# Optimization experiments

Hardware: AMD Instinct MI355X
Metric: run time of the kernel (lower is better)

The kernel has to match this reference:

```python
import jax, jax.numpy as jnp
from jax import lax
import numpy as np

B, CIN, COUT, WDIM, SIN, K = 8, 512, 512, 512, 64, 3
UP, DOWN, TAPS = 2, 2, 12
PX0, PX1, PY0, PY1 = 9, 8, 9, 8  # from StyleGAN3 padding formula for these rates
CLAMP, SLOPE = 256.0, 0.2
GAIN = float(np.sqrt(2.0))
FS_TMP, CUTOFF, HALFW = 128.0, 16.0, 16.0
DN = ('NCHW', 'OIHW', 'NCHW')


def _kaiser_beta(a):
    if a > 50.0:
        return 0.1102 * (a - 8.7)
    if a > 21.0:
        return 0.5842 * (a - 21.0) ** 0.4 + 0.07886 * (a - 21.0)
    return 0.0


def _firwin(numtaps, cutoff, width, fs):
    # replicates scipy.signal.firwin(numtaps, cutoff, width=width, fs=fs)
    nyq = fs / 2.0
    atten = 2.285 * (numtaps - 1) * np.pi * (width / nyq) + 7.95
    beta = _kaiser_beta(atten)
    win = np.kaiser(numtaps, beta)
    m = np.arange(numtaps) - (numtaps - 1) / 2.0
    fc = cutoff / nyq
    h = fc * np.sinc(fc * m) * win
    h /= h.sum()
    return h.astype(np.float32)


def setup_inputs() -> dict:
    key = jax.random.key(0)
    ks = jax.random.split(key, 4)
    f = jnp.asarray(_firwin(TAPS, CUTOFF, 2.0 * HALFW, FS_TMP))
    return {
        'x': jax.random.normal(ks[0], (B, CIN, SIN, SIN), jnp.float32),
        'w': jax.random.normal(ks[1], (B, WDIM), jnp.float32),
        'affine_w': jax.random.normal(ks[2], (CIN, WDIM), jnp.float32),
        'affine_b': jnp.ones((CIN,), jnp.float32),  # bias_init=1
        'conv_w': jax.random.normal(ks[3], (COUT, CIN, K, K), jnp.float32),
        'conv_b': jnp.zeros((COUT,), jnp.float32),
        'up_filter': f,
        'down_filter': f,  # same cutoff/width/fs for in and out here
    }


def _depthwise(x, f1d, axis, stride=1, pad=(0, 0), lhs_dil=1):
    # separable depthwise FIR along one spatial axis (axis 2 = H, 3 = W)
    C, t = x.shape[1], f1d.shape[0]
    if axis == 2:
        k = jnp.broadcast_to(f1d.reshape(1, 1, t, 1), (C, 1, t, 1))
        return lax.conv_general_dilated(x, k, (stride, 1), [pad, (0, 0)],
                                        lhs_dilation=(lhs_dil, 1),
                                        feature_group_count=C, dimension_numbers=DN)
    k = jnp.broadcast_to(f1d.reshape(1, 1, 1, t), (C, 1, 1, t))
    return lax.conv_general_dilated(x, k, (1, stride), [(0, 0), pad],
                                    lhs_dilation=(1, lhs_dil),
                                    feature_group_count=C, dimension_numbers=DN)


def reference(x, w, affine_w, affine_b, conv_w, conv_b, up_filter, down_filter):
    # --- affine: FullyConnectedLayer(w_dim, in_channels, bias_init=1) ---
    styles = w @ (affine_w.T * (1.0 / np.sqrt(WDIM))) + affine_b  # [B, CIN]
    # --- modulated_conv2d with demodulation (input_gain = ema.rsqrt() = 1) ---
    wt = conv_w * lax.rsqrt(jnp.mean(conv_w ** 2, axis=(1, 2, 3), keepdims=True))
    s = styles * lax.rsqrt(jnp.mean(styles ** 2))
    ww = wt[None] * s[:, None, :, None, None]                     # [B,COUT,CIN,K,K]
    ww = ww * lax.rsqrt(jnp.sum(ww ** 2, axis=(2, 3, 4)) + 1e-8)[:, :, None, None, None]
    conv1 = lambda xi, wi: lax.conv_general_dilated(
        xi[None], wi, (1, 1), [(K - 1, K - 1)] * 2, dimension_numbers=DN)[0]
    x = jax.vmap(conv1)(x, ww)                                    # [B,COUT,66,66]
    # --- filtered_lrelu: bias -> upfirdn(up) -> lrelu*gain, clamp -> upfirdn(down) ---
    x = x + conv_b[None, :, None, None]
    fu = up_filter[::-1] * UP  # flip_filter=False; per-pass gain = up (total up^2)
    x = _depthwise(x, fu, 2, pad=(PY0, PY1 + UP - 1), lhs_dil=UP)
    x = _depthwise(x, fu, 3, pad=(PX0, PX1 + UP - 1), lhs_dil=UP)  # [B,COUT,138,138]
    x = jnp.clip(jnp.where(x >= 0, x, SLOPE * x) * GAIN, -CLAMP, CLAMP)
    fd = down_filter[::-1]
    x = _depthwise(x, fd, 2, stride=DOWN)
    x = _depthwise(x, fd, 3, stride=DOWN)                          # [B,COUT,64,64]
    return x
```

## Files before the change

kernel.cpp:

```cpp
#include <hip/hip_runtime.h>

typedef __attribute__((ext_vector_type(4))) float floatx4;
typedef __attribute__((ext_vector_type(8))) short short8;

#define AS1(p) ((const __attribute__((address_space(1))) unsigned int*)(p))
#define AS3(p) ((__attribute__((address_space(3))) unsigned int*)(p))

static __device__ __forceinline__ void async16(const void* g, void* l) {
  __builtin_amdgcn_global_load_lds(AS1(g), AS3(l), 16, 0, 0);
}

static __device__ __forceinline__ unsigned short f2bf(float f) {
  unsigned u = __float_as_uint(f);
  unsigned r = u + 0x7FFFu + ((u >> 16) & 1u);
  return (unsigned short)(r >> 16);
}
static __device__ __forceinline__ float bf2f(unsigned short h) {
  return __uint_as_float(((unsigned)h) << 16);
}
static __device__ __forceinline__ float bf_lo(unsigned u) { return __uint_as_float(u << 16); }
static __device__ __forceinline__ float bf_hi(unsigned u) { return __uint_as_float(u & 0xFFFF0000u); }

static __device__ __forceinline__ float actf(float v) {
  float a = v >= 0.f ? v : 0.2f * v;
  a *= 1.41421356237309515f;
  return fminf(fmaxf(a, -256.f), 256.f);
}

__global__ void k_styles(const float* __restrict__ w, const float* __restrict__ aw,
                         const float* __restrict__ ab, float* __restrict__ styles) {
  int t = blockIdx.x * 256 + threadIdx.x;
  int b = t >> 9, c = t & 511;
  float acc = 0.f;
  for (int d = 0; d < 512; ++d) acc += w[b * 512 + d] * aw[c * 512 + d];
  styles[t] = acc * 0.04419417382415922f + ab[c];
}

__global__ void k_msr(const float* __restrict__ styles, float* __restrict__ msr) {
  __shared__ float red[256];
  float acc = 0.f;
  for (int i = threadIdx.x; i < 4096; i += 256) { float v = styles[i]; acc += v * v; }
  red[threadIdx.x] = acc; __syncthreads();
  for (int s = 128; s > 0; s >>= 1) {
    if ((int)threadIdx.x < s) red[threadIdx.x] += red[threadIdx.x + s];
    __syncthreads();
  }
  if (threadIdx.x == 0) *msr = rsqrtf(red[0] / 4096.0f);
}

__global__ void k_wstat(const float* __restrict__ cw, float* __restrict__ t, float* __restrict__ q) {
  int o = blockIdx.x, tid = threadIdx.x;
  __shared__ float red[256];
  float tot = 0.f;
  for (int i = tid; i < 512; i += 256) {
    const float* p = cw + ((size_t)o * 512 + i) * 9;
    float s = 0.f;
#pragma unroll
    for (int k = 0; k < 9; ++k) s += p[k] * p[k];
    q[o * 512 + i] = s;
    tot += s;
  }
  red[tid] = tot; __syncthreads();
  for (int s2 = 128; s2 > 0; s2 >>= 1) {
    if (tid < s2) red[tid] += red[tid + s2];
    __syncthreads();
  }
  if (tid == 0) t[o] = rsqrtf(red[0] / 4608.0f);
}

__global__ void k_dmod(const float* __restrict__ styles, const float* __restrict__ msr,
                       const float* __restrict__ t, const float* __restrict__ q,
                       float* __restrict__ g) {
  int idx = blockIdx.x * 256 + threadIdx.x;
  int b = idx >> 9, o = idx & 511;
  float m = *msr;
  float acc = 0.f;
  for (int i = 0; i < 512; ++i) {
    float s = styles[b * 512 + i] * m;
    acc += s * s * q[o * 512 + i];
  }
  float to = t[o];
  g[idx] = to * rsqrtf(to * to * acc + 1e-8f);
}

__global__ __launch_bounds__(256) void k_wpack(const float* __restrict__ cw,
                                               const float* __restrict__ styles,
                                               const float* __restrict__ msr,
                                               const float* __restrict__ g,
                                               unsigned short* __restrict__ wbf2) {
  __shared__ float raw[512][11];
  int o = blockIdx.x, tid = threadIdx.x;
  for (int i = tid; i < 512; i += 256) {
    const float* p = cw + ((size_t)o * 512 + i) * 9;
#pragma unroll
    for (int k = 0; k < 9; ++k) raw[i][k] = p[k];
  }
  __syncthreads();
  float m = *msr;
  const int nb = o >> 7, wn = (o >> 6) & 1, ni = (o >> 4) & 3, ol = o & 15;
  for (int b = 0; b < 8; ++b) {
    float gg = g[b * 512 + o];
    const size_t base_bo = ((size_t)(b * 4 + nb) * 2 + wn);
    for (int f = tid; f < 9 * 512; f += 256) {
      int s = f >> 9, i = f & 511;
      int ic = i >> 5, qq = (i >> 3) & 3, j = i & 7;
      float v = raw[i][s] * gg * (styles[b * 512 + i] * m);
      size_t idx = ((((base_bo * 9 + s) * 16 + ic) * 4 + ni) * 512) + (qq * 16 + ol) * 8 + j;
      wbf2[idx] = f2bf(v);
    }
  }
}

__global__ __launch_bounds__(256) void k_xpack(const float* __restrict__ x,
                                               unsigned short* __restrict__ xp) {
  __shared__ float tile[64][65];
  int Y = blockIdx.x, cc0 = blockIdx.y * 64, b = blockIdx.z;
  int tid = threadIdx.x;
  int yy = Y - 2;
  bool valid = (yy >= 0 && yy < 64);
  if (valid) {
    for (int it = 0; it < 16; ++it) {
      int f = it * 256 + tid;
      int cc = f >> 6, xx = f & 63;
      tile[xx][cc] = x[(((size_t)b * 512 + cc0 + cc) * 64 + yy) * 64 + xx];
    }
  }
  __syncthreads();
  for (int it = 0; it < 17; ++it) {
    int f = it * 256 + tid;
    int X = f >> 6, cc = f & 63;
    int xx = X - 2;
    float v = (valid && xx >= 0 && xx < 64) ? tile[xx][cc] : 0.f;
    xp[(((size_t)b * 68 + Y) * 68 + X) * 512 + cc0 + cc] = f2bf(v);
  }
}

__global__ __launch_bounds__(256, 2) void k_conv(const unsigned short* __restrict__ xp,
                                                 const unsigned short* __restrict__ wbf2,
                                                 const float* __restrict__ cb,
                                                 float* __restrict__ y) {
  __shared__ __align__(16) unsigned short lds[24576];
  const int tid = threadIdx.x;
  const int w = tid >> 6, lane = tid & 63;
  const int wm = w & 1, wn = w >> 1;
  const int q = lane >> 4, ln = lane & 15;

  const int xcd = blockIdx.x & 7;
  const int slot = blockIdx.x >> 3;
  const int combo = xcd * 4 + slot / 35;
  const int mt = slot % 35;
  const int nt = combo & 3;
  const int b = combo >> 2;
  const int m0 = mt * 128, n0 = nt * 128;
  const int oy0 = m0 / 66;

  const unsigned short* xpb = xp + (size_t)b * (68 * 68 * 512);

  size_t gof_p[6];
#pragma unroll
  for (int i = 0; i < 6; ++i) {
    int pv = w * 96 + i * 16 + (lane >> 2);
    int pve = pv < 339 ? pv : 339;
    int r = pve / 68, px = pve - r * 68;
    int Y = oy0 + r; if (Y > 67) Y = 67;
    int ch = ((lane & 3) ^ ((pve >> 1) & 3)) * 8;
    gof_p[i] = (size_t)(Y * 68 + px) * 512 + ch;
  }

  int pvA[4];
#pragma unroll
  for (int mi = 0; mi < 4; ++mi) {
    int p = m0 + wm * 64 + mi * 16 + ln; if (p > 4355) p = 4355;
    int oy = p / 66, ox = p - oy * 66;
    pvA[mi] = (oy - oy0) * 68 + ox;
  }

  const unsigned short* wB = wbf2 + (((size_t)(b * 4 + nt) * 2 + wn) * 294912) + (size_t)lane * 8;

  floatx4 acc[4][4];
#pragma unroll
  for (int i = 0; i < 4; ++i)
#pragma unroll
    for (int j = 0; j < 4; ++j) acc[i][j] = (floatx4){0.f, 0.f, 0.f, 0.f};

  unsigned short* pat0 = lds;
  unsigned short* pat1 = lds + 12288;

#pragma unroll
  for (int i = 0; i < 6; ++i)
    async16(xpb + gof_p[i], pat0 + (w * 96 + i * 16) * 32);

  short8 bF[4];
#pragma unroll
  for (int ni = 0; ni < 4; ++ni)
    bF[ni] = *(const short8*)(wB + ni * 512);

  for (int ic = 0; ic < 16; ++ic) {
    asm volatile("s_waitcnt vmcnt(0)" ::: "memory");
    asm volatile("s_barrier" ::: "memory");
    const unsigned short* pb = (ic & 1) ? pat1 : pat0;
    unsigned short* pn = (ic & 1) ? pat0 : pat1;
    const size_t pchan = (size_t)(ic + 1) * 32;
#pragma unroll
    for (int s = 0; s < 9; ++s) {
      if (s >= 1 && s <= 6 && ic < 15)
        async16(xpb + gof_p[s - 1] + pchan, pn + (w * 96 + (s - 1) * 16) * 32);
      const int sn = (s < 8) ? s + 1 : 0;
      const int icn = (s < 8) ? ic : (ic < 15 ? ic + 1 : 15);
      const unsigned short* wBn = wB + ((size_t)sn * 16 + icn) * 2048;
      short8 bN[4];
#pragma unroll
      for (int ni = 0; ni < 4; ++ni) bN[ni] = *(const short8*)(wBn + ni * 512);
      const int d = (s / 3) * 68 + (s % 3);
      short8 aF[4];
#pragma unroll
      for (int mi = 0; mi < 4; ++mi) {
        int pv = pvA[mi] + d;
        int off = pv * 32 + ((q ^ ((pv >> 1) & 3)) << 3);
        aF[mi] = *(const short8*)(pb + off);
      }
#pragma unroll
      for (int mi = 0; mi < 4; ++mi)
#pragma unroll
        for (int ni = 0; ni < 4; ++ni)
          acc[mi][ni] = __builtin_amdgcn_mfma_f32_16x16x32_bf16(aF[mi], bF[ni], acc[mi][ni], 0, 0, 0);
#pragma unroll
      for (int ni = 0; ni < 4; ++ni) bF[ni] = bN[ni];
    }
  }

  __syncthreads();
  float* slab = (float*)lds + w * 2176;
  const int pbase = m0 + wm * 64;
  const bool pok = (pbase + ln * 4) < 4356;
  float cbv[4];
#pragma unroll
  for (int ni = 0; ni < 4; ++ni) cbv[ni] = cb[n0 + wn * 64 + ni * 16 + ln];

#pragma unroll
  for (int pass = 0; pass < 2; ++pass) {
#pragma unroll
    for (int ni2 = 0; ni2 < 2; ++ni2) {
      const int ni = pass * 2 + ni2;
#pragma unroll
      for (int mi = 0; mi < 4; ++mi) {
        float4 v;
        v.x = acc[mi][ni][0] + cbv[ni];
        v.y = acc[mi][ni][1] + cbv[ni];
        v.z = acc[mi][ni][2] + cbv[ni];
        v.w = acc[mi][ni][3] + cbv[ni];
        *(float4*)&slab[(ni2 * 16 + ln) * 68 + mi * 16 + q * 4] = v;
      }
    }
#pragma unroll
    for (int i = 0; i < 8; ++i) {
      const int orow = i * 4 + q;
      const int o = n0 + wn * 64 + pass * 32 + orow;
      if (pok) {
        float4 vv = *(const float4*)&slab[orow * 68 + ln * 4];
        *(float4*)&y[((size_t)b * 512 + o) * 4356 + pbase + ln * 4] = vv;
      }
    }
  }
}

__global__ __launch_bounds__(256) void k_updown(const float* __restrict__ yg,
                                                const float* __restrict__ uf,
                                                const float* __restrict__ df,
                                                float* __restrict__ out) {
  __shared__ __align__(16) unsigned short t1t2[64 * 144];
  __shared__ __align__(16) unsigned short zbuf[138 * 144];
  const int tid = threadIdx.x;
  const int plane = blockIdx.x;
  const float* yp = yg + (size_t)plane * 4356;
  float fuw[12], fdw[12];
#pragma unroll
  for (int i = 0; i < 12; ++i) { fuw[i] = uf[11 - i] * 2.0f; fdw[i] = df[11 - i]; }

  for (int t = tid; t < 69 * 66; t += 256) {
    int v = t / 66, xx = t - v * 66;
    float ae = 0.f, ao = 0.f;
#pragma unroll
    for (int u = 0; u < 6; ++u) {
      int r = v + u - 4;
      float yv = (r >= 0 && r < 66) ? yp[r * 66 + xx] : 0.f;
      ae += yv * fuw[2 * u + 1];
      ao += yv * fuw[2 * u];
    }
    t1t2[(2 * v) * 66 + xx] = f2bf(ae);
    t1t2[(2 * v + 1) * 66 + xx] = f2bf(ao);
  }
  __syncthreads();

  for (int t = tid; t < 138 * 69; t += 256) {
    int Y = t / 69, h = t - Y * 69;
    float ae = 0.f, ao = 0.f;
#pragma unroll
    for (int u = 0; u < 6; ++u) {
      int c = h + u - 4;
      float tv = (c >= 0 && c < 66) ? bf2f(t1t2[Y * 66 + c]) : 0.f;
      ae += tv * fuw[2 * u + 1];
      ao += tv * fuw[2 * u];
    }
    ae = actf(ae); ao = actf(ao);
    unsigned pack = (unsigned)f2bf(ae) | ((unsigned)f2bf(ao) << 16);
    *(unsigned*)&zbuf[Y * 144 + 2 * h] = pack;
  }
  __syncthreads();

  for (int t = tid; t < 64 * 18; t += 256) {
    int yr = t / 18, cx = t - yr * 18;
    int X0 = cx * 8;
    float acc[8];
#pragma unroll
    for (int e = 0; e < 8; ++e) acc[e] = 0.f;
#pragma unroll
    for (int i = 0; i < 12; ++i) {
      uint4 zv = *(const uint4*)&zbuf[(2 * yr + i) * 144 + X0];
      float c = fdw[i];
      acc[0] += c * bf_lo(zv.x); acc[1] += c * bf_hi(zv.x);
      acc[2] += c * bf_lo(zv.y); acc[3] += c * bf_hi(zv.y);
      acc[4] += c * bf_lo(zv.z); acc[5] += c * bf_hi(zv.z);
      acc[6] += c * bf_lo(zv.w); acc[7] += c * bf_hi(zv.w);
    }
    uint4 st;
    st.x = (unsigned)f2bf(acc[0]) | ((unsigned)f2bf(acc[1]) << 16);
    st.y = (unsigned)f2bf(acc[2]) | ((unsigned)f2bf(acc[3]) << 16);
    st.z = (unsigned)f2bf(acc[4]) | ((unsigned)f2bf(acc[5]) << 16);
    st.w = (unsigned)f2bf(acc[6]) | ((unsigned)f2bf(acc[7]) << 16);
    *(uint4*)&t1t2[yr * 144 + X0] = st;
  }
  __syncthreads();

  for (int t = tid; t < 4096; t += 256) {
    int yr = t >> 6, xx = t & 63;
    float acc = 0.f;
#pragma unroll
    for (int j = 0; j < 12; j += 2) {
      unsigned pv = *(const unsigned*)&t1t2[yr * 144 + 2 * xx + j];
      acc += fdw[j] * bf_lo(pv) + fdw[j + 1] * bf_hi(pv);
    }
    out[(size_t)plane * 4096 + t] = acc;
  }
}

extern "C" void kernel_launch(void* const* d_in, const int* in_sizes, int n_in,
                              void* d_out, int out_size, void* d_ws, size_t ws_size,
                              hipStream_t stream) {
  const float* x  = (const float*)d_in[0];
  const float* w  = (const float*)d_in[1];
  const float* aw = (const float*)d_in[2];
  const float* ab = (const float*)d_in[3];
  const float* cw = (const float*)d_in[4];
  const float* cb = (const float*)d_in[5];
  const float* uf = (const float*)d_in[6];
  const float* df = (const float*)d_in[7];
  float* out = (float*)d_out;
  char* ws = (char*)d_ws;

  float* styles = (float*)(ws + 0);
  float* msr    = (float*)(ws + 16384);
  float* tbuf   = (float*)(ws + 16640);
  float* qbuf   = (float*)(ws + 18688);
  float* gbuf   = (float*)(ws + 1067264);
  unsigned short* xp   = (unsigned short*)(ws + 1083648);
  unsigned short* wbf2 = (unsigned short*)(ws + 38963456);
  float* yb            = (float*)(ws + 76712192);

  k_styles<<<16, 256, 0, stream>>>(w, aw, ab, styles);
  k_msr<<<1, 256, 0, stream>>>(styles, msr);
  k_wstat<<<512, 256, 0, stream>>>(cw, tbuf, qbuf);
  k_dmod<<<16, 256, 0, stream>>>(styles, msr, tbuf, qbuf, gbuf);
  k_wpack<<<512, 256, 0, stream>>>(cw, styles, msr, gbuf, wbf2);
  k_xpack<<<dim3(68, 8, 8), 256, 0, stream>>>(x, xp);
  k_conv<<<1120, 256, 0, stream>>>(xp, wbf2, cb, yb);
  k_updown<<<4096, 256, 0, stream>>>(yb, uf, df, out);
}
```

Measured before the change: 657.5 us.

## Split updown planes into column halves with register-blocked FIR passes

The up/down filter kernel now handles half of each plane's output columns per block, doubling the grid. It stages the input tile in LDS with halo and computes 8 outputs per thread in each FIR pass using vectorized LDS reads. The activation gain is folded into the second up-filter's coefficients. Shared memory per block shrinks, which allows four blocks per CU under the new launch bounds. The cost is redundant halo computation at the column split, plus higher register pressure from the 8-wide accumulators.

```diff
diff --git a/kernel.cpp b/kernel.cpp
--- a/kernel.cpp
+++ b/kernel.cpp
@@ -15,17 +15,17 @@
   unsigned r = u + 0x7FFFu + ((u >> 16) & 1u);
   return (unsigned short)(r >> 16);
 }
+static __device__ __forceinline__ unsigned packbf(float lo, float hi) {
+  unsigned ul = __float_as_uint(lo), uh = __float_as_uint(hi);
+  ul = ul + 0x7FFFu + ((ul >> 16) & 1u);
+  uh = uh + 0x7FFFu + ((uh >> 16) & 1u);
+  return (ul >> 16) | (uh & 0xFFFF0000u);
+}
 static __device__ __forceinline__ float bf2f(unsigned short h) {
   return __uint_as_float(((unsigned)h) << 16);
 }
 static __device__ __forceinline__ float bf_lo(unsigned u) { return __uint_as_float(u << 16); }
 static __device__ __forceinline__ float bf_hi(unsigned u) { return __uint_as_float(u & 0xFFFF0000u); }
-
-static __device__ __forceinline__ float actf(float v) {
-  float a = v >= 0.f ? v : 0.2f * v;
-  a *= 1.41421356237309515f;
-  return fminf(fmaxf(a, -256.f), 256.f);
-}
 
 __global__ void k_styles(const float* __restrict__ w, const float* __restrict__ aw,
                          const float* __restrict__ ab, float* __restrict__ styles) {
@@ -264,59 +264,120 @@
   }
 }
 
-__global__ __launch_bounds__(256) void k_updown(const float* __restrict__ yg,
-                                                const float* __restrict__ uf,
-                                                const float* __restrict__ df,
-                                                float* __restrict__ out) {
-  __shared__ __align__(16) unsigned short t1t2[64 * 144];
-  __shared__ __align__(16) unsigned short zbuf[138 * 144];
+__global__ __launch_bounds__(256, 4) void k_updown(const float* __restrict__ yg,
+                                                   const float* __restrict__ uf,
+                                                   const float* __restrict__ df,
+                                                   float* __restrict__ out) {
+  __shared__ __align__(16) unsigned short zraw[138 * 88];
+  __shared__ __align__(16) unsigned short t1buf[138 * 56];
   const int tid = threadIdx.x;
-  const int plane = blockIdx.x;
+  const int plane = blockIdx.x >> 1;
+  const int s = blockIdx.x & 1;
   const float* yp = yg + (size_t)plane * 4356;
-  float fuw[12], fdw[12];
-#pragma unroll
-  for (int i = 0; i < 12; ++i) { fuw[i] = uf[11 - i] * 2.0f; fdw[i] = df[11 - i]; }
-
-  for (int t = tid; t < 69 * 66; t += 256) {
-    int v = t / 66, xx = t - v * 66;
-    float ae = 0.f, ao = 0.f;
+
+  float fub[12], fuc[12], fdw[12];
+#pragma unroll
+  for (int i = 0; i < 12; ++i) {
+    float u = uf[11 - i] * 2.0f;
+    fub[i] = u;
+    fuc[i] = u * 1.41421356237309515f;
+    fdw[i] = df[11 - i];
+  }
+
+  float* ybuf = (float*)zraw;
+  const int xoff = 32 * s - 4;
+  for (int t = tid; t < 75 * 48; t += 256) {
+    int row = t / 48, col = t - row * 48;
+    int r = row - 4, x = xoff + col;
+    float v = (r >= 0 && r < 66 && x >= 0 && x < 66) ? yp[r * 66 + x] : 0.f;
+    ybuf[t] = v;
+  }
+  __syncthreads();
+
+  for (int t = tid; t < 69 * 6; t += 256) {
+    int v = t / 6, c = t - v * 6;
+    float ae[8], ao[8];
+#pragma unroll
+    for (int e = 0; e < 8; ++e) { ae[e] = 0.f; ao[e] = 0.f; }
 #pragma unroll
     for (int u = 0; u < 6; ++u) {
-      int r = v + u - 4;
-      float yv = (r >= 0 && r < 66) ? yp[r * 66 + xx] : 0.f;
-      ae += yv * fuw[2 * u + 1];
-      ao += yv * fuw[2 * u];
-    }
-    t1t2[(2 * v) * 66 + xx] = f2bf(ae);
-    t1t2[(2 * v + 1) * 66 + xx] = f2bf(ao);
-  }
-  __syncthreads();
-
-  for (int t = tid; t < 138 * 69; t += 256) {
-    int Y = t / 69, h = t - Y * 69;
-    float ae = 0.f, ao = 0.f;
+      const float* yr = &ybuf[(v + u) * 48 + 8 * c];
+      float4 p0 = *(const float4*)yr;
+      float4 p1 = *(const float4*)(yr + 4);
+      float fe = fub[2 * u + 1], fo = fub[2 * u];
+      ae[0] += p0.x * fe; ao[0] += p0.x * fo;
+      ae[1] += p0.y * fe; ao[1] += p0.y * fo;
+      ae[2] += p0.z * fe; ao[2] += p0.z * fo;
+      ae[3] += p0.w * fe; ao[3] += p0.w * fo;
+      ae[4] += p1.x * fe; ao[4] += p1.x * fo;
+      ae[5] += p1.y * fe; ao[5] += p1.y * fo;
+      ae[6] += p1.z * fe; ao[6] += p1.z * fo;
+      ae[7] += p1.w * fe; ao[7] += p1.w * fo;
+    }
+    uint4 se, so;
+    se.x = packbf(ae[0], ae[1]); se.y = packbf(ae[2], ae[3]);
+    se.z = packbf(ae[4], ae[5]); se.w = packbf(ae[6], ae[7]);
+    so.x = packbf(ao[0], ao[1]); so.y = packbf(ao[2], ao[3]);
+    so.z = packbf(ao[4], ao[5]); so.w = packbf(ao[6], ao[7]);
+    *(uint4*)&t1buf[(2 * v) * 56 + 8 * c] = se;
+    *(uint4*)&t1buf[(2 * v + 1) * 56 + 8 * c] = so;
+  }
+  __syncthreads();
+
+  for (int t = tid; t < 138 * 5; t += 256) {
+    int Y = t / 5, k = t - Y * 5;
+    const unsigned short* tr = &t1buf[Y * 56 + 8 * k];
+    uint4 r0 = *(const uint4*)tr;
+    uint4 r1 = *(const uint4*)(tr + 8);
+    float a[14];
+    a[0] = bf_lo(r0.x);  a[1] = bf_hi(r0.x);
+    a[2] = bf_lo(r0.y);  a[3] = bf_hi(r0.y);
+    a[4] = bf_lo(r0.z);  a[5] = bf_hi(r0.z);
+    a[6] = bf_lo(r0.w);  a[7] = bf_hi(r0.w);
+    a[8] = bf_lo(r1.x);  a[9] = bf_hi(r1.x);
+    a[10] = bf_lo(r1.y); a[11] = bf_hi(r1.y);
+    a[12] = bf_lo(r1.z); a[13] = bf_hi(r1.z);
+    float ae[8], ao[8];
+#pragma unroll
+    for (int p = 0; p < 8; ++p) { ae[p] = 0.f; ao[p] = 0.f; }
 #pragma unroll
     for (int u = 0; u < 6; ++u) {
-      int c = h + u - 4;
-      float tv = (c >= 0 && c < 66) ? bf2f(t1t2[Y * 66 + c]) : 0.f;
-      ae += tv * fuw[2 * u + 1];
-      ao += tv * fuw[2 * u];
-    }
-    ae = actf(ae); ao = actf(ao);
-    unsigned pack = (unsigned)f2bf(ae) | ((unsigned)f2bf(ao) << 16);
-    *(unsigned*)&zbuf[Y * 144 + 2 * h] = pack;
-  }
-  __syncthreads();
-
-  for (int t = tid; t < 64 * 18; t += 256) {
-    int yr = t / 18, cx = t - yr * 18;
-    int X0 = cx * 8;
+      float fe = fuc[2 * u + 1], fo = fuc[2 * u];
+#pragma unroll
+      for (int p = 0; p < 8; ++p) {
+        float tv = a[p + u];
+        ae[p] += tv * fe;
+        ao[p] += tv * fo;
+      }
+    }
+    uint4 s0, s1;
+    float ze[8], zo[8];
+#pragma unroll
+    for (int p = 0; p < 8; ++p) {
+      float v0 = fmaxf(ae[p], 0.f) + 0.2f * fminf(ae[p], 0.f);
+      float v1 = fmaxf(ao[p], 0.f) + 0.2f * fminf(ao[p], 0.f);
+      ze[p] = fminf(fmaxf(v0, -256.f), 256.f);
+      zo[p] = fminf(fmaxf(v1, -256.f), 256.f);
+    }
+    s0.x = packbf(ze[0], zo[0]); s0.y = packbf(ze[1], zo[1]);
+    s0.z = packbf(ze[2], zo[2]); s0.w = packbf(ze[3], zo[3]);
+    s1.x = packbf(ze[4], zo[4]); s1.y = packbf(ze[5], zo[5]);
+    s1.z = packbf(ze[6], zo[6]); s1.w = packbf(ze[7], zo[7]);
+    unsigned short* zr = &zraw[Y * 88 + 16 * k];
+    *(uint4*)zr = s0;
+    *(uint4*)(zr + 8) = s1;
+  }
+  __syncthreads();
+
+  unsigned short* t2 = t1buf;
+  for (int t = tid; t < 64 * 10; t += 256) {
+    int yr = t / 10, k = t - yr * 10;
     float acc[8];
 #pragma unroll
     for (int e = 0; e < 8; ++e) acc[e] = 0.f;
 #pragma unroll
     for (int i = 0; i < 12; ++i) {
-      uint4 zv = *(const uint4*)&zbuf[(2 * yr + i) * 144 + X0];
+      uint4 zv = *(const uint4*)&zraw[(2 * yr + i) * 88 + 8 * k];
       float c = fdw[i];
       acc[0] += c * bf_lo(zv.x); acc[1] += c * bf_hi(zv.x);
       acc[2] += c * bf_lo(zv.y); acc[3] += c * bf_hi(zv.y);
@@ -324,23 +385,45 @@
       acc[6] += c * bf_lo(zv.w); acc[7] += c * bf_hi(zv.w);
     }
     uint4 st;
-    st.x = (unsigned)f2bf(acc[0]) | ((unsigned)f2bf(acc[1]) << 16);
-    st.y = (unsigned)f2bf(acc[2]) | ((unsigned)f2bf(acc[3]) << 16);
-    st.z = (unsigned)f2bf(acc[4]) | ((unsigned)f2bf(acc[5]) << 16);
-    st.w = (unsigned)f2bf(acc[6]) | ((unsigned)f2bf(acc[7]) << 16);
-    *(uint4*)&t1t2[yr * 144 + X0] = st;
-  }
-  __syncthreads();
-
-  for (int t = tid; t < 4096; t += 256) {
-    int yr = t >> 6, xx = t & 63;
-    float acc = 0.f;
-#pragma unroll
-    for (int j = 0; j < 12; j += 2) {
-      unsigned pv = *(const unsigned*)&t1t2[yr * 144 + 2 * xx + j];
-      acc += fdw[j] * bf_lo(pv) + fdw[j + 1] * bf_hi(pv);
-    }
-    out[(size_t)plane * 4096 + t] = acc;
+    st.x = packbf(acc[0], acc[1]); st.y = packbf(acc[2], acc[3]);
+    st.z = packbf(acc[4], acc[5]); st.w = packbf(acc[6], acc[7]);
+    *(uint4*)&t2[yr * 88 + 8 * k] = st;
+  }
+  __syncthreads();
+
+  {
+    int t = tid;
+    int yr = t >> 2, ce = t & 3;
+    const unsigned short* tr = &t2[yr * 88 + 16 * ce];
+    uint4 q0 = *(const uint4*)tr;
+    uint4 q1 = *(const uint4*)(tr + 8);
+    uint4 q2 = *(const uint4*)(tr + 16);
+    uint4 q3 = *(const uint4*)(tr + 24);
+    float wv[26];
+    wv[0] = bf_lo(q0.x);  wv[1] = bf_hi(q0.x);
+    wv[2] = bf_lo(q0.y);  wv[3] = bf_hi(q0.y);
+    wv[4] = bf_lo(q0.z);  wv[5] = bf_hi(q0.z);
+    wv[6] = bf_lo(q0.w);  wv[7] = bf_hi(q0.w);
+    wv[8] = bf_lo(q1.x);  wv[9] = bf_hi(q1.x);
+    wv[10] = bf_lo(q1.y); wv[11] = bf_hi(q1.y);
+    wv[12] = bf_lo(q1.z); wv[13] = bf_hi(q1.z);
+    wv[14] = bf_lo(q1.w); wv[15] = bf_hi(q1.w);
+    wv[16] = bf_lo(q2.x); wv[17] = bf_hi(q2.x);
+    wv[18] = bf_lo(q2.y); wv[19] = bf_hi(q2.y);
+    wv[20] = bf_lo(q2.z); wv[21] = bf_hi(q2.z);
+    wv[22] = bf_lo(q2.w); wv[23] = bf_hi(q2.w);
+    wv[24] = bf_lo(q3.x); wv[25] = bf_hi(q3.x);
+    float ov[8];
+#pragma unroll
+    for (int e = 0; e < 8; ++e) {
+      float acc = 0.f;
+#pragma unroll
+      for (int j = 0; j < 12; ++j) acc += fdw[j] * wv[2 * e + j];
+      ov[e] = acc;
+    }
+    float* op = out + (size_t)plane * 4096 + yr * 64 + 32 * s + 8 * ce;
+    *(float4*)op = (float4){ov[0], ov[1], ov[2], ov[3]};
+    *(float4*)(op + 4) = (float4){ov[4], ov[5], ov[6], ov[7]};
   }
 }
 
@@ -374,5 +457,5 @@
   k_wpack<<<512, 256, 0, stream>>>(cw, styles, msr, gbuf, wbf2);
   k_xpack<<<dim3(68, 8, 8), 256, 0, stream>>>(x, xp);
   k_conv<<<1120, 256, 0, stream>>>(xp, wbf2, cb, yb);
-  k_updown<<<4096, 256, 0, stream>>>(yb, uf, df, out);
-}
+  k_updown<<<8192, 256, 0, stream>>>(yb, uf, df, out);
+}
```

Result: faster. 539.5 us (-17.9%).
